# Optimization experiments

Hardware: AMD Instinct MI355X
Metric: run time of the kernel (lower is better)

## Reference

```python
import jax, jax.numpy as jnp
import numpy as np

B, N, D = 2, 2048, 256
H = 8
HD = D // H
SCALE = HD ** 0.5  # NOTE: source MULTIPLIES by sqrt(head_dim)
EPS = 1e-5
DFF = 4 * D


def setup_inputs() -> dict:
    key = jax.random.key(0)
    ks = jax.random.split(key, 9)
    s = lambda fan_in: 1.0 / np.sqrt(fan_in)
    return {
        "x": jax.random.normal(ks[0], (B, N, D), dtype=jnp.float32),
        # weights stored [in, out] (transposed torch Linear)
        "qkv_w": jax.random.normal(ks[1], (D, 3 * D), dtype=jnp.float32) * s(D),
        "proj_w": jax.random.normal(ks[2], (D, D), dtype=jnp.float32) * s(D),
        "proj_b": jax.random.normal(ks[3], (D,), dtype=jnp.float32) * 0.01,
        "fc1_w": jax.random.normal(ks[4], (D, DFF), dtype=jnp.float32) * s(D),
        "fc1_b": jax.random.normal(ks[5], (DFF,), dtype=jnp.float32) * 0.01,
        "fc2_w": jax.random.normal(ks[6], (DFF, D), dtype=jnp.float32) * s(DFF),
        "fc2_b": jax.random.normal(ks[7], (D,), dtype=jnp.float32) * 0.01,
        "ln1_g": jnp.ones((D,), dtype=jnp.float32),
        "ln1_b": jnp.zeros((D,), dtype=jnp.float32),
    }


def _layernorm(x, g, b):
    mu = jnp.mean(x, axis=-1, keepdims=True)
    var = jnp.mean(jnp.square(x - mu), axis=-1, keepdims=True)
    return (x - mu) * jax.lax.rsqrt(var + EPS) * g + b


def reference(x, qkv_w, proj_w, proj_b, fc1_w, fc1_b, fc2_w, fc2_b, ln1_g, ln1_b):
    b, n, d = x.shape
    # --- MHA ---
    qkv = (x @ qkv_w).reshape(b, n, 3, H, HD)
    q = qkv[:, :, 0].transpose(0, 2, 1, 3)  # [B,H,N,HD]
    k = qkv[:, :, 1].transpose(0, 2, 1, 3)
    v = qkv[:, :, 2].transpose(0, 2, 1, 3)
    att = jnp.einsum("bhqd,bhkd->bhqk", q, k) * SCALE  # multiplied, per source
    att = jax.nn.softmax(att, axis=-1)
    out = jnp.einsum("bhqk,bhkd->bhqd", att, v)
    out = out.transpose(0, 2, 1, 3).reshape(b, n, d)
    out = out @ proj_w + proj_b
    # --- post-norm residual ---
    net = _layernorm(out + x, ln1_g, ln1_b)
    shortcut = net
    # --- MLP (NO activation in source forward) ---
    net = (net @ fc1_w + fc1_b) @ fc2_w + fc2_b
    return net + shortcut
```

## Files before the change

### kernel.cpp

```cpp
#include <hip/hip_runtime.h>


typedef __attribute__((ext_vector_type(8))) short short8;
typedef __attribute__((ext_vector_type(8))) _Float16 half8;
typedef __attribute__((ext_vector_type(4))) _Float16 half4;
typedef __attribute__((ext_vector_type(2))) __fp16 fp16x2;
typedef __attribute__((ext_vector_type(4))) float floatx4;
typedef __attribute__((ext_vector_type(2))) unsigned int uint2v;
typedef unsigned short u16;

#define MFMAG(a,b,c)  __builtin_amdgcn_mfma_f32_16x16x32_f16((a),(b),(c),0,0,0)
#if __has_builtin(__builtin_amdgcn_mfma_f32_16x16x16_f16)
#define MFMAPV(a,b,c) __builtin_amdgcn_mfma_f32_16x16x16_f16((a),(b),(c),0,0,0)
#else
#define MFMAPV(a,b,c) __builtin_amdgcn_mfma_f32_16x16x16f16((a),(b),(c),0,0,0)
#endif
#define CLF 8.1615404f

#if __has_builtin(__builtin_amdgcn_exp2f)
#define EX2(x) __builtin_amdgcn_exp2f(x)
#else
#define EX2(x) exp2f(x)
#endif

__device__ __forceinline__ float bf2f(u16 u) { return __uint_as_float(((unsigned)u) << 16); }
__device__ __forceinline__ float h2f(u16 u) { _Float16 h = *(_Float16*)&u; return (float)h; }
__device__ __forceinline__ u16 f2h(float f) { _Float16 h = (_Float16)f; return *(u16*)&h; }
__device__ __forceinline__ unsigned pkh2(float a, float b) {
#if __has_builtin(__builtin_amdgcn_cvt_pkrtz)
  fp16x2 h = __builtin_amdgcn_cvt_pkrtz(a, b);
  return *(unsigned*)&h;
#else
  return (unsigned)f2h(a) | ((unsigned)f2h(b) << 16);
#endif
}
__device__ __forceinline__ void gll16(const void* g, void* l) {
  __builtin_amdgcn_global_load_lds((const __attribute__((address_space(1))) void*)g,
                                   (__attribute__((address_space(3))) void*)l, 16, 0, 0);
}

__global__ __launch_bounds__(256) void prep_k(
    const void* __restrict__ x, const void* __restrict__ qkv_w,
    const void* __restrict__ proj_w, const void* __restrict__ fc1_w,
    const void* __restrict__ fc2_w, const void* __restrict__ proj_b,
    const void* __restrict__ fc1_b, const void* __restrict__ fc2_b,
    const void* __restrict__ ln_g, const void* __restrict__ ln_b,
    u16* __restrict__ x_f, u16* __restrict__ wq_f,
    u16* __restrict__ wt_proj, u16* __restrict__ wt_fc1, u16* __restrict__ wt_fc2,
    u16* __restrict__ b_proj, u16* __restrict__ b_fc1, u16* __restrict__ b_fc2,
    u16* __restrict__ g_ln, u16* __restrict__ bb_ln)
{
  __shared__ u16 tr[64][70];
  const int lane = threadIdx.x & 63;
  const float probe = bf2f(((const u16*)qkv_w)[lane]);
  const bool f32 = __ballot(!(fabsf(probe) < 1000.0f)) != 0ull;
  const int bid = blockIdx.x, tid = threadIdx.x;
  #define RD(p, i) (f32 ? ((const float*)(p))[i] : bf2f(((const u16*)(p))[i]))
  if (bid < 4096) {
    const size_t i = (size_t)bid * 256 + tid;
    x_f[i] = f2h(RD(x, i));
  } else if (bid < 4288) {
    int idx = bid - 4096;
    const void* src; u16* dst; int Ns, Kt, tk, tn;
    if (idx < 48)       { src = qkv_w;  dst = wq_f;    Ns = 768;  Kt = 256;
                          tk = idx & 3;  tn = idx >> 2; }
    else if (idx < 64)  { idx -= 48;  src = proj_w; dst = wt_proj; Ns = 256; Kt = 256;
                          tk = idx & 3;  tn = idx >> 2; }
    else if (idx < 128) { idx -= 64;  src = fc1_w;  dst = wt_fc1;  Ns = 1024; Kt = 256;
                          tk = idx & 3;  tn = idx >> 2; }
    else                { idx -= 128; src = fc2_w;  dst = wt_fc2;  Ns = 256;  Kt = 1024;
                          tk = idx & 15; tn = idx >> 4; }
    const int k0 = tk * 64, n0 = tn * 64;
    const int r = tid >> 6, c = tid & 63;
#pragma unroll
    for (int p = 0; p < 16; ++p) {
      const int k = k0 + p * 4 + r;
      tr[c][p * 4 + r] = f2h(RD(src, (size_t)k * Ns + n0 + c));
    }
    __syncthreads();
#pragma unroll
    for (int p = 0; p < 16; ++p) {
      const int n = n0 + p * 4 + r;
      dst[(size_t)n * Kt + k0 + c] = tr[p * 4 + r][c];
    }
  } else {
    const int j = (bid - 4288) * 256 + tid;
    if (j < 256)       b_proj[j]        = f2h(RD(proj_b, j));
    else if (j < 1280) b_fc1[j - 256]   = f2h(RD(fc1_b, j - 256));
    else if (j < 1536) b_fc2[j - 1280]  = f2h(RD(fc2_b, j - 1280));
    else if (j < 1792) g_ln[j - 1536]   = f2h(RD(ln_g, j - 1536));
    else if (j < 2048) bb_ln[j - 1792]  = f2h(RD(ln_b, j - 1792));
  }
  #undef RD
}

template<int TW, int EPI, bool BIAS, bool RES, bool COMB, bool PF2 = false>
__global__ __launch_bounds__(256) void gemm_k(
    const u16* __restrict__ A, const u16* __restrict__ Bt, const u16* __restrict__ A2,
    const u16* __restrict__ bias, const u16* __restrict__ res,
    void* __restrict__ out0, u16* __restrict__ aux1, u16* __restrict__ aux3,
    const float* __restrict__ muc,
    int M, int Nn, int K)
{
  constexpr int BT = TW * 32;
  constexpr int NC = TW / 2;
  __shared__ __align__(16) u16 As[BT][40];
  __shared__ __align__(16) u16 Bs[BT][40];
  __shared__ __align__(16) u16 Vt[(EPI == 2) ? 64 * 72 : 1];
  const int tid = threadIdx.x;
  const int m0 = blockIdx.y * BT, n0 = blockIdx.x * BT;
  const int wid = tid >> 6, lane = tid & 63;
  const int wm = (wid >> 1) * (TW * 16), wn = (wid & 1) * (TW * 16);
  const int lm = lane & 15, quad = lane >> 4;

  floatx4 zero = {0.f, 0.f, 0.f, 0.f};
  floatx4 acc[TW][TW];
#pragma unroll
  for (int i = 0; i < TW; ++i)
#pragma unroll
    for (int j = 0; j < TW; ++j) acc[i][j] = zero;

  auto comb8 = [&](int t, int col8) -> short8 {
    const size_t o = (size_t)t * 256 + col8;
    const int h = col8 >> 5;
    const float m0_ = muc[t * 8 + h],          m1_ = muc[32768 + t * 8 + h];
    const float m2_ = muc[65536 + t * 8 + h],  m3_ = muc[98304 + t * 8 + h];
    const float M = fmaxf(fmaxf(m0_, m1_), fmaxf(m2_, m3_));
    float w0 = EX2(m0_ - M), w1 = EX2(m1_ - M), w2 = EX2(m2_ - M), w3 = EX2(m3_ - M);
    const float inv = 1.f / (w0 + w1 + w2 + w3);
    w0 *= inv; w1 *= inv; w2 *= inv; w3 *= inv;
    short8 a0 = *(const short8*)&A[o],  a1 = *(const short8*)&A[o + 1048576];
    short8 a2 = *(const short8*)&A2[o], a3 = *(const short8*)&A2[o + 1048576];
    float v[8];
#pragma unroll
    for (int j = 0; j < 8; ++j)
      v[j] = w0 * h2f((u16)a0[j]) + w1 * h2f((u16)a1[j])
           + w2 * h2f((u16)a2[j]) + w3 * h2f((u16)a3[j]);
    uint2v uu0 = {pkh2(v[0], v[1]), pkh2(v[2], v[3])};
    uint2v uu1 = {pkh2(v[4], v[5]), pkh2(v[6], v[7])};
    short8 r;
    *(uint2v*)&r = uu0; *((uint2v*)&r + 1) = uu1;
    return r;
  };

  int srow[NC], soff[NC];
#pragma unroll
  for (int c = 0; c < NC; ++c) {
    const int cid = tid * NC + c;
    srow[c] = cid >> 2; soff[c] = (cid & 3) * 8;
  }

  auto ld = [&](short8* ta, short8* tb, int kk) {
#pragma unroll
    for (int c = 0; c < NC; ++c) {
      tb[c] = *(const short8*)&Bt[(size_t)(n0 + srow[c]) * K + kk + soff[c]];
      if (COMB) ta[c] = comb8(m0 + srow[c], kk + soff[c]);
      else      ta[c] = *(const short8*)&A[(size_t)(m0 + srow[c]) * K + kk + soff[c]];
    }
  };
  auto st = [&](short8* ta, short8* tb) {
#pragma unroll
    for (int c = 0; c < NC; ++c) {
      *(short8*)&As[srow[c]][soff[c]] = ta[c];
      *(short8*)&Bs[srow[c]][soff[c]] = tb[c];
    }
  };
  auto comp = [&]() {
    half8 fa[TW], fb[TW];
#pragma unroll
    for (int t = 0; t < TW; ++t) {
      fa[t] = *(const half8*)&As[wm + t * 16 + lm][quad * 8];
      fb[t] = *(const half8*)&Bs[wn + t * 16 + lm][quad * 8];
    }
#pragma unroll
    for (int i = 0; i < TW; ++i)
#pragma unroll
      for (int j = 0; j < TW; ++j)
        acc[i][j] = MFMAG(fa[i], fb[j], acc[i][j]);
  };

  if (PF2) {
    short8 ra0[NC], rb0[NC], ra1[NC], rb1[NC];
    ld(ra0, rb0, 0);
    ld(ra1, rb1, 32);
    for (int k0 = 0; k0 < K; k0 += 64) {
      if (k0) __syncthreads();
      st(ra0, rb0);
      __syncthreads();
      if (k0 + 64 < K) ld(ra0, rb0, k0 + 64);
      comp();
      __syncthreads();
      st(ra1, rb1);
      __syncthreads();
      if (k0 + 96 < K) ld(ra1, rb1, k0 + 96);
      comp();
    }
  } else {
    short8 ra0[NC], rb0[NC];
    ld(ra0, rb0, 0);
    for (int k0 = 0; k0 < K; k0 += 32) {
      if (k0) __syncthreads();
      st(ra0, rb0);
      __syncthreads();
      if (k0 + 32 < K) ld(ra0, rb0, k0 + 32);
      comp();
    }
  }

  if (EPI == 2 && n0 >= 512) {
    __syncthreads();
#pragma unroll
    for (int i = 0; i < TW; ++i)
#pragma unroll
      for (int j = 0; j < TW; ++j)
#pragma unroll
        for (int r = 0; r < 4; ++r)
          Vt[(wn + j * 16 + lm) * 72 + wm + i * 16 + quad * 4 + r] = f2h(acc[i][j][r]);
    __syncthreads();
    const int bb = m0 >> 11, n = m0 & 2047;
#pragma unroll
    for (int pass = 0; pass < 2; ++pass) {
      const int dl = (tid >> 3) + pass * 32;
      const int oct = tid & 7;
      const int col = n0 - 512 + dl;
      const int d = col & 31, hh = col >> 5;
      short8 v = *(const short8*)&Vt[dl * 72 + oct * 8];
      *(short8*)&((u16*)out0)[(size_t)((bb * 8 + hh) * 32 + d) * 2048 + n + oct * 8] = v;
    }
    return;
  }

#pragma unroll
  for (int i = 0; i < TW; ++i) {
    const int rowb = m0 + wm + i * 16 + quad * 4;
#pragma unroll
    for (int j = 0; j < TW; ++j) {
      const int col = n0 + wn + j * 16 + lm;
      const float bv = BIAS ? h2f(bias[col]) : 0.f;
#pragma unroll
      for (int r = 0; r < 4; ++r) {
        const int row = rowb + r;
        float v = acc[i][j][r] + bv;
        const size_t o = (size_t)row * Nn + col;
        if (RES) v += h2f(res[o]);
        if (EPI == 0) {
          ((float*)out0)[o] = v;
        } else if (EPI == 1) {
          ((u16*)out0)[o] = f2h(v);
        } else {
          if (col < 256) aux1[(size_t)row * 256 + col] = f2h(v);
          else           aux3[(size_t)row * 256 + (col - 256)] = f2h(v);
        }
      }
    }
  }
}

__global__ __launch_bounds__(256) void projln_k(
    const u16* __restrict__ A,
    const u16* __restrict__ A2,
    const u16* __restrict__ Bt,
    const u16* __restrict__ bias,
    const u16* xh,
    const u16* __restrict__ g, const u16* __restrict__ bb,
    const float* __restrict__ muc,
    u16* net)
{
  __shared__ __align__(16) u16 As[16][40];
  __shared__ __align__(16) u16 Bs[256][40];
  __shared__ float ss[4][16], ssq[4][16];
  const int tid = threadIdx.x;
  const int m0 = blockIdx.x * 16;
  const int wid = tid >> 6, lane = tid & 63;
  const int lm = lane & 15, quad = lane >> 4;

  floatx4 zero = {0.f, 0.f, 0.f, 0.f};
  floatx4 acc[4] = {zero, zero, zero, zero};

  auto comb8 = [&](int t, int col8) -> short8 {
    const size_t o = (size_t)t * 256 + col8;
    const int h = col8 >> 5;
    const float m0_ = muc[t * 8 + h],          m1_ = muc[32768 + t * 8 + h];
    const float m2_ = muc[65536 + t * 8 + h],  m3_ = muc[98304 + t * 8 + h];
    const float M = fmaxf(fmaxf(m0_, m1_), fmaxf(m2_, m3_));
    float w0 = EX2(m0_ - M), w1 = EX2(m1_ - M), w2 = EX2(m2_ - M), w3 = EX2(m3_ - M);
    const float inv = 1.f / (w0 + w1 + w2 + w3);
    w0 *= inv; w1 *= inv; w2 *= inv; w3 *= inv;
    short8 a0 = *(const short8*)&A[o],  a1 = *(const short8*)&A[o + 1048576];
    short8 a2 = *(const short8*)&A2[o], a3 = *(const short8*)&A2[o + 1048576];
    float v[8];
#pragma unroll
    for (int j = 0; j < 8; ++j)
      v[j] = w0 * h2f((u16)a0[j]) + w1 * h2f((u16)a1[j])
           + w2 * h2f((u16)a2[j]) + w3 * h2f((u16)a3[j]);
    uint2v uu0 = {pkh2(v[0], v[1]), pkh2(v[2], v[3])};
    uint2v uu1 = {pkh2(v[4], v[5]), pkh2(v[6], v[7])};
    short8 r;
    *(uint2v*)&r = uu0; *((uint2v*)&r + 1) = uu1;
    return r;
  };

  const int arow = lane >> 2, aoff = (lane & 3) * 8;
  int browv[4];
#pragma unroll
  for (int c = 0; c < 4; ++c) browv[c] = wid * 64 + c * 16 + (lane >> 2);
  const int boff = (lane & 3) * 8;

  short8 ra; short8 rb[4];
  if (wid == 0) ra = comb8(m0 + arow, aoff);
#pragma unroll
  for (int c = 0; c < 4; ++c)
    rb[c] = *(const short8*)&Bt[(size_t)browv[c] * 256 + boff];

  for (int k0 = 0; k0 < 256; k0 += 32) {
    if (k0) __syncthreads();
    if (wid == 0) *(short8*)&As[arow][aoff] = ra;
#pragma unroll
    for (int c = 0; c < 4; ++c)
      *(short8*)&Bs[browv[c]][boff] = rb[c];
    __syncthreads();
    if (k0 + 32 < 256) {
      if (wid == 0) ra = comb8(m0 + arow, k0 + 32 + aoff);
#pragma unroll
      for (int c = 0; c < 4; ++c)
        rb[c] = *(const short8*)&Bt[(size_t)browv[c] * 256 + k0 + 32 + boff];
    }
    half8 fa = *(const half8*)&As[lm][quad * 8];
    half8 fb[4];
#pragma unroll
    for (int j = 0; j < 4; ++j)
      fb[j] = *(const half8*)&Bs[wid * 64 + j * 16 + lm][quad * 8];
#pragma unroll
    for (int j = 0; j < 4; ++j)
      acc[j] = MFMAG(fa, fb[j], acc[j]);
  }

  const int colb = wid * 64 + lm;
  float s[4] = {0.f, 0.f, 0.f, 0.f}, sq[4] = {0.f, 0.f, 0.f, 0.f};
  float vout[4][4];
#pragma unroll
  for (int j = 0; j < 4; ++j) {
    const int col = colb + j * 16;
    const float bv = h2f(bias[col]);
#pragma unroll
    for (int r = 0; r < 4; ++r) {
      const int row = quad * 4 + r;
      float v = acc[j][r] + bv + h2f(xh[(size_t)(m0 + row) * 256 + col]);
      vout[j][r] = v;
      s[r] += v; sq[r] += v * v;
    }
  }
#pragma unroll
  for (int d = 1; d < 16; d <<= 1)
#pragma unroll
    for (int r = 0; r < 4; ++r) {
      s[r] += __shfl_xor(s[r], d);
      sq[r] += __shfl_xor(sq[r], d);
    }
  if (lm == 0)
#pragma unroll
    for (int r = 0; r < 4; ++r) { ss[wid][quad * 4 + r] = s[r]; ssq[wid][quad * 4 + r] = sq[r]; }
  __syncthreads();
#pragma unroll
  for (int r = 0; r < 4; ++r) {
    const int row = quad * 4 + r;
    const float ts = ss[0][row] + ss[1][row] + ss[2][row] + ss[3][row];
    const float tq = ssq[0][row] + ssq[1][row] + ssq[2][row] + ssq[3][row];
    const float mean = ts * (1.f / 256.f);
    const float var = tq * (1.f / 256.f) - mean * mean;
    const float is = rsqrtf(var + 1e-5f);
#pragma unroll
    for (int j = 0; j < 4; ++j) {
      const int col = colb + j * 16;
      net[(size_t)(m0 + row) * 256 + col] =
          f2h((vout[j][r] - mean) * is * h2f(g[col]) + h2f(bb[col]));
    }
  }
}

template<int CHUNKS>
__global__ __launch_bounds__(256) void attn_k(
    const u16* __restrict__ qf16, const u16* __restrict__ kf16,
    const u16* __restrict__ vt, u16* __restrict__ outp, u16* __restrict__ out23,
    float* __restrict__ mu)
{
  __shared__ __align__(16) u16 Ks[2][64][32];
  __shared__ __align__(16) u16 Vs[2][32][64];
  const int tid = threadIdx.x, wid = tid >> 6, lane = tid & 63;
  const int lm = lane & 15, quad = lane >> 4;
  const int bid = blockIdx.x;
  const int chunk = (CHUNKS > 1) ? (bid >> 9) : 0;
  const int qblk = bid & 31, bh = (bid >> 5) & 15;
  const int b = bh >> 3, h = bh & 7;
  const int q0 = qblk * 64 + wid * 16;
  const size_t tb = (size_t)b * 2048;
  const int NT = 32 / CHUNKS;
  const int kofs = chunk * (2048 / CHUNKS);

  half8 qh;
  { size_t off = (tb + q0 + lm) * 256 + h * 32 + quad * 8;
    qh = *(const half8*)&qf16[off]; }

  const int kkey = tid >> 2, kg = tid & 3;
  const size_t kb = (tb + kofs + kkey) * 256 + h * 32 + kg * 8;
  const int vd = tid >> 3, vp = tid & 7, vk8 = vp ^ (vd & 7);
  const size_t vb = (size_t)(bh * 32 + vd) * 2048 + kofs + vk8 * 8;

  gll16(kf16 + kb, (u16*)Ks + tid * 8);
  gll16(vt  + vb,  (u16*)Vs + tid * 8);

  float mrun = -1e30f, lrun = 0.f;
  floatx4 o0 = {0.f,0.f,0.f,0.f}, o1 = {0.f,0.f,0.f,0.f};

  for (int kt = 0; kt < NT; ++kt) {
    const int buf = kt & 1;
    __syncthreads();
    if (kt < NT - 1) {
      const int nb = (buf ^ 1) * 2048;
      const size_t ko = (size_t)(kt + 1) * 16384;
      const size_t vo = (size_t)(kt + 1) * 64;
      gll16(kf16 + kb + ko, (u16*)Ks + nb + tid * 8);
      gll16(vt  + vb + vo,  (u16*)Vs + nb + tid * 8);
    }

    floatx4 z[4];
#pragma unroll
    for (int kf = 0; kf < 4; ++kf) {
      half8 khf = *(const half8*)&Ks[buf][kf * 16 + lm][quad * 8];
      floatx4 zz = {0.f,0.f,0.f,0.f};
      z[kf] = MFMAG(khf, qh, zz);
    }
    float zm = fmaxf(fmaxf(fmaxf(z[0][0], z[0][1]), fmaxf(z[0][2], z[0][3])),
               fmaxf(fmaxf(z[1][0], z[1][1]), fmaxf(z[1][2], z[1][3])));
    zm = fmaxf(zm, fmaxf(fmaxf(fmaxf(z[2][0], z[2][1]), fmaxf(z[2][2], z[2][3])),
                   fmaxf(fmaxf(z[3][0], z[3][1]), fmaxf(z[3][2], z[3][3]))));
    zm = fmaxf(zm, __shfl_xor(zm, 16));
    zm = fmaxf(zm, __shfl_xor(zm, 32));
    const float mn = fmaxf(mrun, zm);
    const float alpha = EX2((mrun - mn) * CLF);
    const float mc = mn * CLF;
    mrun = mn;
    float ls = 0.f;
    half4 pb[4];
#pragma unroll
    for (int kf = 0; kf < 4; ++kf) {
      const float p0 = EX2(__builtin_fmaf(z[kf][0], CLF, -mc));
      const float p1 = EX2(__builtin_fmaf(z[kf][1], CLF, -mc));
      const float p2 = EX2(__builtin_fmaf(z[kf][2], CLF, -mc));
      const float p3 = EX2(__builtin_fmaf(z[kf][3], CLF, -mc));
      ls += (p0 + p1) + (p2 + p3);
      uint2v uu = {pkh2(p0, p1), pkh2(p2, p3)};
      pb[kf] = *(half4*)&uu;
    }
    ls += __shfl_xor(ls, 16);
    ls += __shfl_xor(ls, 32);
    lrun = lrun * alpha + ls;
#pragma unroll
    for (int r = 0; r < 4; ++r) { o0[r] *= alpha; o1[r] *= alpha; }
    const u16* vbase = (const u16*)Vs + buf * 2048;
#pragma unroll
    for (int kf = 0; kf < 4; ++kf) {
      const int k8 = 2 * kf + (quad >> 1);
      const int d0 = lm, d1 = 16 + lm;
      half4 vf0 = *(const half4*)(vbase + (d0 * 8 + (k8 ^ (d0 & 7))) * 8 + (quad & 1) * 4);
      half4 vf1 = *(const half4*)(vbase + (d1 * 8 + (k8 ^ (d1 & 7))) * 8 + (quad & 1) * 4);
      o0 = MFMAPV(vf0, pb[kf], o0);
      o1 = MFMAPV(vf1, pb[kf], o1);
    }
  }
  const float inv = 1.0f / lrun;
  const size_t tok = tb + q0 + lm;
  u16* dst = ((CHUNKS > 2 && chunk >= 2) ? out23 : outp) + (size_t)(chunk & 1) * 1048576;
  const size_t rowo = tok * 256 + h * 32;
#pragma unroll
  for (int r = 0; r < 4; ++r) {
    dst[rowo + quad * 4 + r]      = f2h(o0[r] * inv);
    dst[rowo + 16 + quad * 4 + r] = f2h(o1[r] * inv);
  }
  if (CHUNKS > 1 && quad == 0)
    mu[chunk * 32768 + tok * 8 + h] = __builtin_fmaf(mrun, CLF, __log2f(lrun));
}

template<int CHUNKS>
__global__ __launch_bounds__(256) void combine_k(u16* __restrict__ d,
                                                 const u16* __restrict__ e,
                                                 const float* __restrict__ mu)
{
  const int t = blockIdx.x, c = threadIdx.x, h = c >> 5;
  const size_t o = (size_t)t * 256 + c;
  float m[CHUNKS];
  float M = -1e30f;
#pragma unroll
  for (int i = 0; i < CHUNKS; ++i) { m[i] = mu[i * 32768 + t * 8 + h]; M = fmaxf(M, m[i]); }
  float wsum = 0.f, acc = 0.f;
#pragma unroll
  for (int i = 0; i < CHUNKS; ++i) {
    const float w = EX2(m[i] - M);
    const u16 v = (i < 2) ? d[o + (size_t)i * 1048576] : e[o + (size_t)(i - 2) * 1048576];
    wsum += w; acc += w * h2f(v);
  }
  d[o] = f2h(acc / wsum);
}

__global__ __launch_bounds__(256) void ln_k(const float* __restrict__ pf,
                                            const u16* __restrict__ xh,
                                            const u16* __restrict__ g,
                                            const u16* __restrict__ bta,
                                            u16* __restrict__ net)
{
  const int t = blockIdx.x, c = threadIdx.x;
  const size_t o = (size_t)t * 256 + c;
  float v = pf[o] + h2f(xh[o]);
  float s = v, s2 = v * v;
#pragma unroll
  for (int d = 1; d < 64; d <<= 1) { s += __shfl_xor(s, d); s2 += __shfl_xor(s2, d); }
  __shared__ float ss[4], ss2[4];
  const int w = c >> 6;
  if ((c & 63) == 0) { ss[w] = s; ss2[w] = s2; }
  __syncthreads();
  s = ss[0] + ss[1] + ss[2] + ss[3];
  s2 = ss2[0] + ss2[1] + ss2[2] + ss2[3];
  const float mu = s * (1.f / 256.f);
  const float var = s2 * (1.f / 256.f) - mu * mu;
  const float is = rsqrtf(var + 1e-5f);
  net[o] = f2h((v - mu) * is * h2f(g[c]) + h2f(bta[c]));
}

extern "C" void kernel_launch(void* const* d_in, const int* in_sizes, int n_in,
                              void* d_out, int out_size, void* d_ws, size_t ws_size,
                              hipStream_t stream) {
  const void* x      = d_in[0];
  const void* qkv_w  = d_in[1];
  const void* proj_w = d_in[2];
  const void* proj_b = d_in[3];
  const void* fc1_w  = d_in[4];
  const void* fc1_b  = d_in[5];
  const void* fc2_w  = d_in[6];
  const void* fc2_b  = d_in[7];
  const void* ln_g   = d_in[8];
  const void* ln_b   = d_in[9];

  char* ws = (char*)d_ws;
  u16* b_proj  = (u16*)(ws + 4096);
  u16* b_fc1   = (u16*)(ws + 8192);
  u16* b_fc2   = (u16*)(ws + 12288);
  u16* g_ln    = (u16*)(ws + 16384);
  u16* bb_ln   = (u16*)(ws + 20480);
  u16* wq_f    = (u16*)(ws + 131072);
  u16* wt_proj = (u16*)(ws + 524288);
  u16* wt_fc1  = (u16*)(ws + 655360);
  u16* wt_fc2  = (u16*)(ws + 1179648);
  u16* x_f     = (u16*)(ws + 2097152);
  u16* q_f16   = (u16*)(ws + 4194304);
  u16* k_f16   = (u16*)(ws + 6291456);
  u16* vt      = (u16*)(ws + 8388608);
  float* mu    = (float*)(ws + 10485760);
  u16* out23   = (u16*)(ws + 11010048);
  u16* attn    = (u16*)d_out;

  u16* net4    = x_f;
  u16* hbuf4   = (u16*)(ws + 4194304);

  float* projf = (float*)(ws + 4194304);
  u16* net     = (u16*)(ws + 11010048);
  u16* hbuf    = (u16*)(ws + 2097152);

  const bool sk4 = ws_size >= 15204352;
  const bool sk2 = ws_size >= 11010048;

  prep_k<<<4296, 256, 0, stream>>>(x, qkv_w, proj_w, fc1_w, fc2_w,
                                   proj_b, fc1_b, fc2_b, ln_g, ln_b,
                                   x_f, wq_f, wt_proj, wt_fc1, wt_fc2,
                                   b_proj, b_fc1, b_fc2, g_ln, bb_ln);

  gemm_k<2, 2, false, false, false><<<dim3(12, 64), 256, 0, stream>>>(
      x_f, wq_f, nullptr, nullptr, nullptr, vt, q_f16, k_f16, nullptr, 4096, 768, 256);
  if (sk4) {
    attn_k<4><<<2048, 256, 0, stream>>>(q_f16, k_f16, vt, attn, out23, mu);
    projln_k<<<256, 256, 0, stream>>>(attn, out23, wt_proj, b_proj, x_f,
                                      g_ln, bb_ln, mu, net4);
    gemm_k<2, 1, true, false, false><<<dim3(16, 64), 256, 0, stream>>>(
        net4, wt_fc1, nullptr, b_fc1, nullptr, hbuf4, nullptr, nullptr, nullptr,
        4096, 1024, 256);
    gemm_k<2, 0, true, true, false, true><<<dim3(4, 64), 256, 0, stream>>>(
        hbuf4, wt_fc2, nullptr, b_fc2, net4, d_out, nullptr, nullptr, nullptr,
        4096, 256, 1024);
    return;
  }
  if (sk2) {
    attn_k<2><<<1024, 256, 0, stream>>>(q_f16, k_f16, vt, attn, nullptr, mu);
    combine_k<2><<<4096, 256, 0, stream>>>(attn, nullptr, mu);
    gemm_k<2, 0, true, false, false><<<dim3(4, 64), 256, 0, stream>>>(
        attn, wt_proj, nullptr, b_proj, nullptr, projf, nullptr, nullptr, nullptr,
        4096, 256, 256);
  } else {
    attn_k<1><<<512, 256, 0, stream>>>(q_f16, k_f16, vt, attn, nullptr, nullptr);
    gemm_k<2, 0, true, false, false><<<dim3(4, 64), 256, 0, stream>>>(
        attn, wt_proj, nullptr, b_proj, nullptr, projf, nullptr, nullptr, nullptr,
        4096, 256, 256);
  }
  ln_k<<<4096, 256, 0, stream>>>(projf, x_f, g_ln, bb_ln, net);
  gemm_k<2, 1, true, false, false><<<dim3(16, 64), 256, 0, stream>>>(
      net, wt_fc1, nullptr, b_fc1, nullptr, hbuf, nullptr, nullptr, nullptr,
      4096, 1024, 256);
  gemm_k<2, 0, true, true, false><<<dim3(4, 64), 256, 0, stream>>>(
      hbuf, wt_fc2, nullptr, b_fc2, net, d_out, nullptr, nullptr, nullptr,
      4096, 256, 1024);
}
```

Baseline: 144.6 us.

## Use 512-thread blocks for proj+LN and fc2 GEMM, vectorize x conversion

The prep kernel now converts four x elements per thread with a 4-wide packed store, cutting the block count. The fused projection+layernorm kernel and the fc2 GEMM move to 512-thread blocks of eight waves, each owning a smaller slice of output columns, so more waves can hide memory latency. The fc2 path drops the double-buffered PF2 prefetch variant in favour of a dedicated single-prefetch kernel in which half the threads stage A and half stage B. This trades fewer MFMAs per wave for more waves and cross-wave LN reduction over eight slots.

```diff
diff --git a/kernel.cpp b/kernel.cpp
--- a/kernel.cpp
+++ b/kernel.cpp
@@ -2,6 +2,7 @@
 
 
 typedef __attribute__((ext_vector_type(8))) short short8;
+typedef __attribute__((ext_vector_type(4))) short short4v;
 typedef __attribute__((ext_vector_type(8))) _Float16 half8;
 typedef __attribute__((ext_vector_type(4))) _Float16 half4;
 typedef __attribute__((ext_vector_type(2))) __fp16 fp16x2;
@@ -56,11 +57,14 @@
   const bool f32 = __ballot(!(fabsf(probe) < 1000.0f)) != 0ull;
   const int bid = blockIdx.x, tid = threadIdx.x;
   #define RD(p, i) (f32 ? ((const float*)(p))[i] : bf2f(((const u16*)(p))[i]))
-  if (bid < 4096) {
-    const size_t i = (size_t)bid * 256 + tid;
-    x_f[i] = f2h(RD(x, i));
-  } else if (bid < 4288) {
-    int idx = bid - 4096;
+  if (bid < 1024) {
+    const size_t i = (size_t)bid * 1024 + tid * 4;
+    const u16 o0 = f2h(RD(x, i)),     o1 = f2h(RD(x, i + 1));
+    const u16 o2 = f2h(RD(x, i + 2)), o3 = f2h(RD(x, i + 3));
+    short4v sv = {(short)o0, (short)o1, (short)o2, (short)o3};
+    *(short4v*)&x_f[i] = sv;
+  } else if (bid < 1216) {
+    int idx = bid - 1024;
     const void* src; u16* dst; int Ns, Kt, tk, tn;
     if (idx < 48)       { src = qkv_w;  dst = wq_f;    Ns = 768;  Kt = 256;
                           tk = idx & 3;  tn = idx >> 2; }
@@ -84,7 +88,7 @@
       dst[(size_t)n * Kt + k0 + c] = tr[p * 4 + r][c];
     }
   } else {
-    const int j = (bid - 4288) * 256 + tid;
+    const int j = (bid - 1216) * 256 + tid;
     if (j < 256)       b_proj[j]        = f2h(RD(proj_b, j));
     else if (j < 1280) b_fc1[j - 256]   = f2h(RD(fc1_b, j - 256));
     else if (j < 1536) b_fc2[j - 1280]  = f2h(RD(fc2_b, j - 1280));
@@ -94,7 +98,7 @@
   #undef RD
 }
 
-template<int TW, int EPI, bool BIAS, bool RES, bool COMB, bool PF2 = false>
+template<int TW, int EPI, bool BIAS, bool RES, bool COMB>
 __global__ __launch_bounds__(256) void gemm_k(
     const u16* __restrict__ A, const u16* __restrict__ Bt, const u16* __restrict__ A2,
     const u16* __restrict__ bias, const u16* __restrict__ res,
@@ -150,22 +154,25 @@
     srow[c] = cid >> 2; soff[c] = (cid & 3) * 8;
   }
 
-  auto ld = [&](short8* ta, short8* tb, int kk) {
+  short8 ra0[NC], rb0[NC];
+  auto ld = [&](int kk) {
 #pragma unroll
     for (int c = 0; c < NC; ++c) {
-      tb[c] = *(const short8*)&Bt[(size_t)(n0 + srow[c]) * K + kk + soff[c]];
-      if (COMB) ta[c] = comb8(m0 + srow[c], kk + soff[c]);
-      else      ta[c] = *(const short8*)&A[(size_t)(m0 + srow[c]) * K + kk + soff[c]];
+      rb0[c] = *(const short8*)&Bt[(size_t)(n0 + srow[c]) * K + kk + soff[c]];
+      if (COMB) ra0[c] = comb8(m0 + srow[c], kk + soff[c]);
+      else      ra0[c] = *(const short8*)&A[(size_t)(m0 + srow[c]) * K + kk + soff[c]];
     }
   };
-  auto st = [&](short8* ta, short8* tb) {
+  ld(0);
+  for (int k0 = 0; k0 < K; k0 += 32) {
+    if (k0) __syncthreads();
 #pragma unroll
     for (int c = 0; c < NC; ++c) {
-      *(short8*)&As[srow[c]][soff[c]] = ta[c];
-      *(short8*)&Bs[srow[c]][soff[c]] = tb[c];
-    }
-  };
-  auto comp = [&]() {
+      *(short8*)&As[srow[c]][soff[c]] = ra0[c];
+      *(short8*)&Bs[srow[c]][soff[c]] = rb0[c];
+    }
+    __syncthreads();
+    if (k0 + 32 < K) ld(k0 + 32);
     half8 fa[TW], fb[TW];
 #pragma unroll
     for (int t = 0; t < TW; ++t) {
@@ -177,34 +184,6 @@
 #pragma unroll
       for (int j = 0; j < TW; ++j)
         acc[i][j] = MFMAG(fa[i], fb[j], acc[i][j]);
-  };
-
-  if (PF2) {
-    short8 ra0[NC], rb0[NC], ra1[NC], rb1[NC];
-    ld(ra0, rb0, 0);
-    ld(ra1, rb1, 32);
-    for (int k0 = 0; k0 < K; k0 += 64) {
-      if (k0) __syncthreads();
-      st(ra0, rb0);
-      __syncthreads();
-      if (k0 + 64 < K) ld(ra0, rb0, k0 + 64);
-      comp();
-      __syncthreads();
-      st(ra1, rb1);
-      __syncthreads();
-      if (k0 + 96 < K) ld(ra1, rb1, k0 + 96);
-      comp();
-    }
-  } else {
-    short8 ra0[NC], rb0[NC];
-    ld(ra0, rb0, 0);
-    for (int k0 = 0; k0 < K; k0 += 32) {
-      if (k0) __syncthreads();
-      st(ra0, rb0);
-      __syncthreads();
-      if (k0 + 32 < K) ld(ra0, rb0, k0 + 32);
-      comp();
-    }
   }
 
   if (EPI == 2 && n0 >= 512) {
@@ -256,7 +235,57 @@
   }
 }
 
-__global__ __launch_bounds__(256) void projln_k(
+__global__ __launch_bounds__(512) void gemm8_k(
+    const u16* __restrict__ A, const u16* __restrict__ Bt,
+    const u16* __restrict__ bias, const u16* __restrict__ res,
+    float* __restrict__ out0, int Nn, int K)
+{
+  __shared__ __align__(16) u16 As[64][40];
+  __shared__ __align__(16) u16 Bs[64][40];
+  const int tid = threadIdx.x;
+  const int m0 = blockIdx.y * 64, n0 = blockIdx.x * 64;
+  const int wid = tid >> 6, lane = tid & 63;
+  const int wm = (wid & 3) * 16, wn = (wid >> 2) * 32;
+  const int lm = lane & 15, quad = lane >> 4;
+
+  floatx4 zero = {0.f, 0.f, 0.f, 0.f};
+  floatx4 acc0 = zero, acc1 = zero;
+
+  const int sgrp = tid >> 8, stid = tid & 255;
+  const int srow = stid >> 2, soff = (stid & 3) * 8;
+  const u16* sp = sgrp ? Bt : A;
+  const int sbase = sgrp ? n0 : m0;
+
+  short8 rr;
+  rr = *(const short8*)&sp[(size_t)(sbase + srow) * K + soff];
+  for (int k0 = 0; k0 < K; k0 += 32) {
+    if (k0) __syncthreads();
+    if (sgrp) *(short8*)&Bs[srow][soff] = rr;
+    else      *(short8*)&As[srow][soff] = rr;
+    __syncthreads();
+    if (k0 + 32 < K)
+      rr = *(const short8*)&sp[(size_t)(sbase + srow) * K + k0 + 32 + soff];
+    half8 fa = *(const half8*)&As[wm + lm][quad * 8];
+    half8 fb0 = *(const half8*)&Bs[wn + lm][quad * 8];
+    half8 fb1 = *(const half8*)&Bs[wn + 16 + lm][quad * 8];
+    acc0 = MFMAG(fa, fb0, acc0);
+    acc1 = MFMAG(fa, fb1, acc1);
+  }
+
+  const int rowb = m0 + wm + quad * 4;
+  const int col0 = n0 + wn + lm, col1 = col0 + 16;
+  const float bv0 = h2f(bias[col0]), bv1 = h2f(bias[col1]);
+#pragma unroll
+  for (int r = 0; r < 4; ++r) {
+    const int row = rowb + r;
+    const size_t o0 = (size_t)row * Nn + col0;
+    const size_t o1 = (size_t)row * Nn + col1;
+    out0[o0] = acc0[r] + bv0 + h2f(res[o0]);
+    out0[o1] = acc1[r] + bv1 + h2f(res[o1]);
+  }
+}
+
+__global__ __launch_bounds__(512) void projln8_k(
     const u16* __restrict__ A,
     const u16* __restrict__ A2,
     const u16* __restrict__ Bt,
@@ -268,14 +297,14 @@
 {
   __shared__ __align__(16) u16 As[16][40];
   __shared__ __align__(16) u16 Bs[256][40];
-  __shared__ float ss[4][16], ssq[4][16];
+  __shared__ float ss[8][16], ssq[8][16];
   const int tid = threadIdx.x;
   const int m0 = blockIdx.x * 16;
   const int wid = tid >> 6, lane = tid & 63;
   const int lm = lane & 15, quad = lane >> 4;
 
   floatx4 zero = {0.f, 0.f, 0.f, 0.f};
-  floatx4 acc[4] = {zero, zero, zero, zero};
+  floatx4 acc0 = zero, acc1 = zero;
 
   auto comb8 = [&](int t, int col8) -> short8 {
     const size_t o = (size_t)t * 256 + col8;
@@ -301,54 +330,42 @@
   };
 
   const int arow = lane >> 2, aoff = (lane & 3) * 8;
-  int browv[4];
-#pragma unroll
-  for (int c = 0; c < 4; ++c) browv[c] = wid * 64 + c * 16 + (lane >> 2);
+  int brow0 = wid * 32 + (lane >> 2), brow1 = brow0 + 16;
   const int boff = (lane & 3) * 8;
 
-  short8 ra; short8 rb[4];
+  short8 ra, rb0, rb1;
   if (wid == 0) ra = comb8(m0 + arow, aoff);
-#pragma unroll
-  for (int c = 0; c < 4; ++c)
-    rb[c] = *(const short8*)&Bt[(size_t)browv[c] * 256 + boff];
+  rb0 = *(const short8*)&Bt[(size_t)brow0 * 256 + boff];
+  rb1 = *(const short8*)&Bt[(size_t)brow1 * 256 + boff];
 
   for (int k0 = 0; k0 < 256; k0 += 32) {
     if (k0) __syncthreads();
     if (wid == 0) *(short8*)&As[arow][aoff] = ra;
-#pragma unroll
-    for (int c = 0; c < 4; ++c)
-      *(short8*)&Bs[browv[c]][boff] = rb[c];
+    *(short8*)&Bs[brow0][boff] = rb0;
+    *(short8*)&Bs[brow1][boff] = rb1;
     __syncthreads();
     if (k0 + 32 < 256) {
       if (wid == 0) ra = comb8(m0 + arow, k0 + 32 + aoff);
-#pragma unroll
-      for (int c = 0; c < 4; ++c)
-        rb[c] = *(const short8*)&Bt[(size_t)browv[c] * 256 + k0 + 32 + boff];
+      rb0 = *(const short8*)&Bt[(size_t)brow0 * 256 + k0 + 32 + boff];
+      rb1 = *(const short8*)&Bt[(size_t)brow1 * 256 + k0 + 32 + boff];
     }
     half8 fa = *(const half8*)&As[lm][quad * 8];
-    half8 fb[4];
-#pragma unroll
-    for (int j = 0; j < 4; ++j)
-      fb[j] = *(const half8*)&Bs[wid * 64 + j * 16 + lm][quad * 8];
-#pragma unroll
-    for (int j = 0; j < 4; ++j)
-      acc[j] = MFMAG(fa, fb[j], acc[j]);
-  }
-
-  const int colb = wid * 64 + lm;
-  float s[4] = {0.f, 0.f, 0.f, 0.f}, sq[4] = {0.f, 0.f, 0.f, 0.f};
-  float vout[4][4];
-#pragma unroll
-  for (int j = 0; j < 4; ++j) {
-    const int col = colb + j * 16;
-    const float bv = h2f(bias[col]);
-#pragma unroll
-    for (int r = 0; r < 4; ++r) {
-      const int row = quad * 4 + r;
-      float v = acc[j][r] + bv + h2f(xh[(size_t)(m0 + row) * 256 + col]);
-      vout[j][r] = v;
-      s[r] += v; sq[r] += v * v;
-    }
+    half8 fb0 = *(const half8*)&Bs[wid * 32 + lm][quad * 8];
+    half8 fb1 = *(const half8*)&Bs[wid * 32 + 16 + lm][quad * 8];
+    acc0 = MFMAG(fa, fb0, acc0);
+    acc1 = MFMAG(fa, fb1, acc1);
+  }
+
+  const int col0 = wid * 32 + lm, col1 = col0 + 16;
+  const float bv0 = h2f(bias[col0]), bv1 = h2f(bias[col1]);
+  float s[4], sq[4], v0[4], v1[4];
+#pragma unroll
+  for (int r = 0; r < 4; ++r) {
+    const int row = quad * 4 + r;
+    const float a = acc0[r] + bv0 + h2f(xh[(size_t)(m0 + row) * 256 + col0]);
+    const float b = acc1[r] + bv1 + h2f(xh[(size_t)(m0 + row) * 256 + col1]);
+    v0[r] = a; v1[r] = b;
+    s[r] = a + b; sq[r] = a * a + b * b;
   }
 #pragma unroll
   for (int d = 1; d < 16; d <<= 1)
@@ -364,17 +381,16 @@
 #pragma unroll
   for (int r = 0; r < 4; ++r) {
     const int row = quad * 4 + r;
-    const float ts = ss[0][row] + ss[1][row] + ss[2][row] + ss[3][row];
-    const float tq = ssq[0][row] + ssq[1][row] + ssq[2][row] + ssq[3][row];
+    float ts = 0.f, tq = 0.f;
+#pragma unroll
+    for (int w = 0; w < 8; ++w) { ts += ss[w][row]; tq += ssq[w][row]; }
     const float mean = ts * (1.f / 256.f);
     const float var = tq * (1.f / 256.f) - mean * mean;
     const float is = rsqrtf(var + 1e-5f);
-#pragma unroll
-    for (int j = 0; j < 4; ++j) {
-      const int col = colb + j * 16;
-      net[(size_t)(m0 + row) * 256 + col] =
-          f2h((vout[j][r] - mean) * is * h2f(g[col]) + h2f(bb[col]));
-    }
+    net[(size_t)(m0 + row) * 256 + col0] =
+        f2h((v0[r] - mean) * is * h2f(g[col0]) + h2f(bb[col0]));
+    net[(size_t)(m0 + row) * 256 + col1] =
+        f2h((v1[r] - mean) * is * h2f(g[col1]) + h2f(bb[col1]));
   }
 }
 
@@ -568,7 +584,7 @@
   const bool sk4 = ws_size >= 15204352;
   const bool sk2 = ws_size >= 11010048;
 
-  prep_k<<<4296, 256, 0, stream>>>(x, qkv_w, proj_w, fc1_w, fc2_w,
+  prep_k<<<1224, 256, 0, stream>>>(x, qkv_w, proj_w, fc1_w, fc2_w,
                                    proj_b, fc1_b, fc2_b, ln_g, ln_b,
                                    x_f, wq_f, wt_proj, wt_fc1, wt_fc2,
                                    b_proj, b_fc1, b_fc2, g_ln, bb_ln);
@@ -577,14 +593,13 @@
       x_f, wq_f, nullptr, nullptr, nullptr, vt, q_f16, k_f16, nullptr, 4096, 768, 256);
   if (sk4) {
     attn_k<4><<<2048, 256, 0, stream>>>(q_f16, k_f16, vt, attn, out23, mu);
-    projln_k<<<256, 256, 0, stream>>>(attn, out23, wt_proj, b_proj, x_f,
-                                      g_ln, bb_ln, mu, net4);
+    projln8_k<<<256, 512, 0, stream>>>(attn, out23, wt_proj, b_proj, x_f,
+                                       g_ln, bb_ln, mu, net4);
     gemm_k<2, 1, true, false, false><<<dim3(16, 64), 256, 0, stream>>>(
         net4, wt_fc1, nullptr, b_fc1, nullptr, hbuf4, nullptr, nullptr, nullptr,
         4096, 1024, 256);
-    gemm_k<2, 0, true, true, false, true><<<dim3(4, 64), 256, 0, stream>>>(
-        hbuf4, wt_fc2, nullptr, b_fc2, net4, d_out, nullptr, nullptr, nullptr,
-        4096, 256, 1024);
+    gemm8_k<<<dim3(4, 64), 512, 0, stream>>>(
+        hbuf4, wt_fc2, b_fc2, net4, (float*)d_out, 256, 1024);
     return;
   }
   if (sk2) {
```

Measured after the change: 144.5 us. No clear change (-0.0%).
